# Optimization experiments

Measured on AMD Instinct MI355X. Metric: run time of the kernel, lower is better.

## Reference

```python
import jax, jax.numpy as jnp
import numpy as np

N_HEAD = 16
N_EMBD = 1024
B, T = 4, 1024


def setup_inputs() -> dict:
    key = jax.random.key(0)
    ks = jax.random.split(key, 8)
    hs = N_EMBD // N_HEAD
    x = jax.random.normal(ks[0], (B, T, N_EMBD), dtype=jnp.float32)
    # previous-layer attention load per token, ~O(1/T) like a softmax column mean
    refractory_state = jax.random.uniform(ks[1], (B, T), dtype=jnp.float32) / T
    s_attn = 1.0 / np.sqrt(N_EMBD)
    W_attn = jax.random.normal(ks[2], (N_EMBD, 3 * N_EMBD), dtype=jnp.float32) * s_attn
    b_attn = jnp.zeros((3 * N_EMBD,), dtype=jnp.float32)
    W_proj = jax.random.normal(ks[3], (N_EMBD, N_EMBD), dtype=jnp.float32) * s_attn
    b_proj = jnp.zeros((N_EMBD,), dtype=jnp.float32)
    # learnable LIF params, init per module (lif_mode='refractory')
    threshold = jnp.full((N_HEAD,), 0.01, dtype=jnp.float32)
    leak = jnp.full((N_HEAD,), 2.0, dtype=jnp.float32)
    steepness = jnp.full((N_HEAD,), 2.0, dtype=jnp.float32)
    ref_strength = jnp.full((N_HEAD,), -2.0, dtype=jnp.float32)
    cross_w = jnp.full((N_HEAD,), -2.0, dtype=jnp.float32)
    return {
        "x": x, "refractory_state": refractory_state,
        "W_attn": W_attn, "b_attn": b_attn,
        "W_proj": W_proj, "b_proj": b_proj,
        "threshold": threshold, "leak": leak, "steepness": steepness,
        "ref_strength": ref_strength, "cross_w": cross_w,
    }


def reference(x, refractory_state, W_attn, b_attn, W_proj, b_proj,
              threshold, leak, steepness, ref_strength, cross_w):
    Bq, Tq, C = x.shape
    H = N_HEAD
    hs = C // H
    qkv = x @ W_attn + b_attn                     # [B,T,3C]
    q, k, v = jnp.split(qkv, 3, axis=-1)
    q = q.reshape(Bq, Tq, H, hs).transpose(0, 2, 1, 3)  # [B,H,T,hs]
    k = k.reshape(Bq, Tq, H, hs).transpose(0, 2, 1, 3)
    v = v.reshape(Bq, Tq, H, hs).transpose(0, 2, 1, 3)

    att = jnp.einsum('bhqd,bhkd->bhqk', q, k) * (1.0 / jnp.sqrt(jnp.asarray(hs, x.dtype)))
    causal = jnp.tril(jnp.ones((Tq, Tq), dtype=bool))
    att = jnp.where(causal[None, None], att, -jnp.inf)
    probs = jax.nn.softmax(att, axis=-1)          # [B,H,T,T]

    thr = (jnp.abs(threshold) * 0.1)[None, :, None, None]
    lk = jax.nn.sigmoid(leak)[None, :, None, None]
    st = jax.nn.softplus(steepness)[None, :, None, None]
    # refractory: column load over queries + cross-layer load
    column_load = probs.mean(axis=-2, keepdims=True)          # [B,H,1,T]
    eff_thr = thr + jax.nn.softplus(ref_strength)[None, :, None, None] * column_load
    eff_thr = eff_thr + jax.nn.sigmoid(cross_w)[None, :, None, None] * refractory_state[:, None, None, :]

    fire = jax.nn.sigmoid(st * (probs - eff_thr))
    lif_w = fire + lk * (1.0 - fire)
    mod = probs * lif_w
    mod = mod / (mod.sum(axis=-1, keepdims=True) + 1e-8)
    new_refractory = mod.mean(axis=1).mean(axis=-2)           # [B,T]

    y = jnp.einsum('bhqk,bhkd->bhqd', mod, v)
    y = y.transpose(0, 2, 1, 3).reshape(Bq, Tq, C)
    y = y @ W_proj + b_proj
    return y, new_refractory
```

## Files before the change

### kernel.cpp

```cpp
#include <hip/hip_runtime.h>
#include <math.h>

#define B_  4
#define T_  1024
#define C_  1024
#define H_  16
#define HS_ 64
#define K2E 0.1803368801f
#define LOG2E 1.44269504f

typedef _Float16 f16;
typedef _Float16 f16x8 __attribute__((ext_vector_type(8)));
typedef float f32x4 __attribute__((ext_vector_type(4)));

#define MFMA16(a,b,c) __builtin_amdgcn_mfma_f32_16x16x32_f16(a,b,c,0,0,0)
#define EXP2(x) __builtin_amdgcn_exp2f(x)
#define RCP(x)  __builtin_amdgcn_rcpf(x)

__device__ __forceinline__ float qsum_(float v){
    v += __shfl_xor(v,1,64); v += __shfl_xor(v,2,64);
    v += __shfl_xor(v,4,64); v += __shfl_xor(v,8,64);
    return v;
}
__device__ __forceinline__ float sigmoidf_(float x){ return 1.0f/(1.0f + __expf(-x)); }
__device__ __forceinline__ float softplusf_(float x){ return fmaxf(x, 0.0f) + log1pf(__expf(-fabsf(x))); }

__global__ __launch_bounds__(256) void conv_f16_k(
    const float* __restrict__ in, f16* __restrict__ out, int n8)
{
    int i = blockIdx.x*256 + threadIdx.x;
    if (i < n8){
        const float4* p = (const float4*)in + (size_t)i*2;
        float4 a = p[0], b = p[1];
        f16x8 o;
        o[0]=(f16)a.x; o[1]=(f16)a.y; o[2]=(f16)a.z; o[3]=(f16)a.w;
        o[4]=(f16)b.x; o[5]=(f16)b.y; o[6]=(f16)b.z; o[7]=(f16)b.w;
        *((f16x8*)out + i) = o;
    }
}

__global__ __launch_bounds__(256) void transpose_f16_k(
    const float* __restrict__ in, f16* __restrict__ out, int K, int N)
{
    __shared__ float tl[32][33];
    const int n0 = blockIdx.x*32, k0 = blockIdx.y*32;
    const int c = threadIdx.x & 31, r4 = threadIdx.x >> 5;
    #pragma unroll
    for (int i=0;i<4;i++){
        int r = r4*4 + i;
        tl[r][c] = in[(size_t)(k0+r)*N + n0 + c];
    }
    __syncthreads();
    #pragma unroll
    for (int i=0;i<4;i++){
        int r = r4*4 + i;
        out[(size_t)(n0+r)*K + k0 + c] = (f16)tl[c][r];
    }
}

__global__ __launch_bounds__(256) void gemm_qkv_k(
    const f16* __restrict__ A, const f16* __restrict__ Bt,
    const float* __restrict__ bias,
    f16* __restrict__ Qh, f16* __restrict__ Kh, f16* __restrict__ Vt)
{
    __shared__ __align__(16) f16 Al[4*1032];
    __shared__ __align__(16) f16 Bl[4*1032];
    const int tid = threadIdx.x;
    const int lane = tid & 63, wave = tid >> 6;
    const int lx = lane & 15, quad = lane >> 4;
    const int wm = wave & 1, wn = wave >> 1;
    const int m0 = blockIdx.y*128, n0 = blockIdx.x*128;
    f32x4 acc[4][4];
    #pragma unroll
    for (int i=0;i<4;i++){
        #pragma unroll
        for (int j=0;j<4;j++){ acc[i][j][0]=0.f;acc[i][j][1]=0.f;acc[i][j][2]=0.f;acc[i][j][3]=0.f; }
    }
    for (int k0=0; k0<1024; k0+=32){
        __syncthreads();
        #pragma unroll
        for (int i=0;i<2;i++){
            int g = i*256 + tid;
            int m = g >> 2, kc = g & 3;
            *(f16x8*)&Al[kc*1032 + m*8] = *(const f16x8*)(A  + (size_t)(m0+m)*1024 + k0 + kc*8);
            *(f16x8*)&Bl[kc*1032 + m*8] = *(const f16x8*)(Bt + (size_t)(n0+m)*1024 + k0 + kc*8);
        }
        __syncthreads();
        f16x8 af[4], bf[4];
        #pragma unroll
        for (int mt=0;mt<4;mt++) af[mt] = *(const f16x8*)&Al[quad*1032 + (wm*64+mt*16+lx)*8];
        #pragma unroll
        for (int nt=0;nt<4;nt++) bf[nt] = *(const f16x8*)&Bl[quad*1032 + (wn*64+nt*16+lx)*8];
        #pragma unroll
        for (int mt=0;mt<4;mt++){
            #pragma unroll
            for (int nt=0;nt<4;nt++)
                acc[mt][nt] = MFMA16(af[mt], bf[nt], acc[mt][nt]);
        }
    }
    #pragma unroll
    for (int mt=0;mt<4;mt++){
        #pragma unroll
        for (int nt=0;nt<4;nt++){
            int n = n0 + wn*64 + nt*16 + lx;
            int which = n >> 10, cc = n & 1023, h = cc >> 6, d = cc & 63;
            float bv = bias[n];
            #pragma unroll
            for (int r=0;r<4;r++){
                int m = m0 + wm*64 + mt*16 + quad*4 + r;
                int bb = m >> 10, t = m & 1023;
                int bh = bb*16 + h;
                float v = acc[mt][nt][r] + bv;
                if (which==0)      Qh[((size_t)bh*1024 + t)*64 + d] = (f16)v;
                else if (which==1) Kh[((size_t)bh*1024 + t)*64 + d] = (f16)v;
                else               Vt[((size_t)bh*64 + d)*1024 + t] = (f16)v;
            }
        }
    }
}

__global__ __launch_bounds__(256) void gemm_proj_k(
    const f16* __restrict__ A, const f16* __restrict__ Bt,
    const float* __restrict__ bias, float* __restrict__ out)
{
    __shared__ __align__(16) f16 Al[4*1032];
    __shared__ __align__(16) f16 Bl[4*1032];
    const int tid = threadIdx.x;
    const int lane = tid & 63, wave = tid >> 6;
    const int lx = lane & 15, quad = lane >> 4;
    const int wm = wave & 1, wn = wave >> 1;
    const int m0 = blockIdx.y*128, n0 = blockIdx.x*128;
    f32x4 acc[4][4];
    #pragma unroll
    for (int i=0;i<4;i++){
        #pragma unroll
        for (int j=0;j<4;j++){ acc[i][j][0]=0.f;acc[i][j][1]=0.f;acc[i][j][2]=0.f;acc[i][j][3]=0.f; }
    }
    for (int k0=0; k0<1024; k0+=32){
        __syncthreads();
        #pragma unroll
        for (int i=0;i<2;i++){
            int g = i*256 + tid;
            int m = g >> 2, kc = g & 3;
            *(f16x8*)&Al[kc*1032 + m*8] = *(const f16x8*)(A  + (size_t)(m0+m)*1024 + k0 + kc*8);
            *(f16x8*)&Bl[kc*1032 + m*8] = *(const f16x8*)(Bt + (size_t)(n0+m)*1024 + k0 + kc*8);
        }
        __syncthreads();
        f16x8 af[4], bf[4];
        #pragma unroll
        for (int mt=0;mt<4;mt++) af[mt] = *(const f16x8*)&Al[quad*1032 + (wm*64+mt*16+lx)*8];
        #pragma unroll
        for (int nt=0;nt<4;nt++) bf[nt] = *(const f16x8*)&Bl[quad*1032 + (wn*64+nt*16+lx)*8];
        #pragma unroll
        for (int mt=0;mt<4;mt++){
            #pragma unroll
            for (int nt=0;nt<4;nt++)
                acc[mt][nt] = MFMA16(af[mt], bf[nt], acc[mt][nt]);
        }
    }
    #pragma unroll
    for (int mt=0;mt<4;mt++){
        #pragma unroll
        for (int nt=0;nt<4;nt++){
            int n = n0 + wn*64 + nt*16 + lx;
            float bv = bias[n];
            #pragma unroll
            for (int r=0;r<4;r++){
                int m = m0 + wm*64 + mt*16 + quad*4 + r;
                out[(size_t)m*1024 + n] = acc[mt][nt][r] + bv;
            }
        }
    }
}

__global__ __launch_bounds__(256) void attn_stats_k(
    const f16* __restrict__ Qh, const f16* __restrict__ Kh,
    float* __restrict__ rowl, float* __restrict__ colp)
{
    __shared__ __align__(16) f16 Kl[8*520];
    __shared__ float colacc[64];
    const int tid = threadIdx.x;
    const int lane = tid & 63, wave = tid >> 6;
    const int lx = lane & 15, quad = lane >> 4;
    const int pair = blockIdx.x >> 6;
    const int bh = blockIdx.x & 63;
    const int qpos = wave*16 + quad*4;

    #pragma unroll 1
    for (int gi=0; gi<2; gi++){
        const int g = gi ? (15-pair) : pair;
        const size_t qoff = ((size_t)bh*1024 + g*64 + wave*16 + lx)*64;
        f16x8 aq0 = *(const f16x8*)(Qh + qoff + quad*8);
        f16x8 aq1 = *(const f16x8*)(Qh + qoff + 32 + quad*8);

        float ls[4] = {0.f,0.f,0.f,0.f};
        for (int kt=0; kt<=g; kt++){
            __syncthreads();
            #pragma unroll
            for (int i=0;i<2;i++){
                int gix = i*256 + tid;
                int key = gix >> 3, kc = gix & 7;
                *(f16x8*)&Kl[kc*520 + key*8] =
                    *(const f16x8*)(Kh + ((size_t)bh*1024 + kt*64 + key)*64 + kc*8);
            }
            __syncthreads();
            const bool diag = (kt == g);
            #pragma unroll
            for (int nt=0;nt<4;nt++){
                f32x4 sc = {0.f,0.f,0.f,0.f};
                f16x8 b0 = *(const f16x8*)&Kl[quad*520     + (nt*16+lx)*8];
                f16x8 b1 = *(const f16x8*)&Kl[(4+quad)*520 + (nt*16+lx)*8];
                sc = MFMA16(aq0, b0, sc);
                sc = MFMA16(aq1, b1, sc);
                #pragma unroll
                for (int r=0;r<4;r++){
                    float sv = sc[r];
                    if (diag && (nt*16+lx) > (qpos + r)) sv = -1e4f;
                    ls[r] += EXP2(sv*K2E);
                }
            }
        }
        float invl[4];
        #pragma unroll
        for (int r=0;r<4;r++){
            float l = qsum_(ls[r]);
            if (lx == 0) rowl[(size_t)bh*1024 + g*64 + qpos + r] = l;
            invl[r] = RCP(l);
        }

        for (int kt=0; kt<=g; kt++){
            __syncthreads();
            #pragma unroll
            for (int i=0;i<2;i++){
                int gix = i*256 + tid;
                int key = gix >> 3, kc = gix & 7;
                *(f16x8*)&Kl[kc*520 + key*8] =
                    *(const f16x8*)(Kh + ((size_t)bh*1024 + kt*64 + key)*64 + kc*8);
            }
            if (tid < 64) colacc[tid] = 0.f;
            __syncthreads();
            const bool diag = (kt == g);
            #pragma unroll
            for (int nt=0;nt<4;nt++){
                f32x4 sc = {0.f,0.f,0.f,0.f};
                f16x8 b0 = *(const f16x8*)&Kl[quad*520     + (nt*16+lx)*8];
                f16x8 b1 = *(const f16x8*)&Kl[(4+quad)*520 + (nt*16+lx)*8];
                sc = MFMA16(aq0, b0, sc);
                sc = MFMA16(aq1, b1, sc);
                float csum = 0.f;
                #pragma unroll
                for (int r=0;r<4;r++){
                    float sv = sc[r];
                    if (diag && (nt*16+lx) > (qpos + r)) sv = -1e4f;
                    csum += EXP2(sv*K2E) * invl[r];
                }
                csum += __shfl_xor(csum,16,64); csum += __shfl_xor(csum,32,64);
                if (quad == 0) atomicAdd(&colacc[nt*16+lx], csum);
            }
            __syncthreads();
            if (tid < 64) atomicAdd(&colp[(size_t)bh*1024 + kt*64 + tid], colacc[tid]);
        }
    }
}

__global__ __launch_bounds__(256) void attn_apply_k(
    const f16* __restrict__ Qh, const f16* __restrict__ Kh, const f16* __restrict__ Vt,
    const float* __restrict__ rowl,
    const float* __restrict__ colp, const float* __restrict__ refr,
    const float* __restrict__ threshold, const float* __restrict__ leak,
    const float* __restrict__ steepness, const float* __restrict__ ref_strength,
    const float* __restrict__ cross_w,
    f16* __restrict__ Yh, float* __restrict__ racc)
{
    __shared__ __align__(16) f16 Kl[8*520];
    __shared__ __align__(16) f16 Vl[8*520];
    __shared__ __align__(16) f16 Pl[4][16*72];
    __shared__ float eb[1024];
    __shared__ float colacc[64];
    const int tid = threadIdx.x;
    const int lane = tid & 63, wave = tid >> 6;
    const int lx = lane & 15, quad = lane >> 4;
    const int pair = blockIdx.x >> 6;
    const int bh = blockIdx.x & 63;
    const int b  = bh >> 4, h = bh & 15;
    const int qpos = wave*16 + quad*4;

    const float thr = fabsf(threshold[h])*0.1f;
    const float lk  = sigmoidf_(leak[h]);
    const float st2 = softplusf_(steepness[h]) * LOG2E;
    const float sprT= softplusf_(ref_strength[h]) * (1.0f/T_);
    const float cw  = sigmoidf_(cross_w[h]);
    const float Alk = 1.f - lk;

    {
        float4 cp = *(const float4*)(colp + (size_t)bh*1024 + tid*4);
        float4 rf = *(const float4*)(refr + (size_t)b*1024 + tid*4);
        eb[tid*4+0] = thr + sprT*cp.x + cw*rf.x;
        eb[tid*4+1] = thr + sprT*cp.y + cw*rf.y;
        eb[tid*4+2] = thr + sprT*cp.z + cw*rf.z;
        eb[tid*4+3] = thr + sprT*cp.w + cw*rf.w;
    }

    #pragma unroll 1
    for (int gi=0; gi<2; gi++){
        const int g = gi ? (15-pair) : pair;
        const size_t qoff = ((size_t)bh*1024 + g*64 + wave*16 + lx)*64;
        f16x8 aq0 = *(const f16x8*)(Qh + qoff + quad*8);
        f16x8 aq1 = *(const f16x8*)(Qh + qoff + 32 + quad*8);

        float invl[4];
        #pragma unroll
        for (int r=0;r<4;r++)
            invl[r] = RCP(rowl[(size_t)bh*1024 + g*64 + qpos + r]);

        f32x4 y[4];
        #pragma unroll
        for (int i=0;i<4;i++){ y[i][0]=0.f;y[i][1]=0.f;y[i][2]=0.f;y[i][3]=0.f; }
        float Dp[4] = {0.f,0.f,0.f,0.f};

        for (int kt=0; kt<=g; kt++){
            __syncthreads();
            #pragma unroll
            for (int i=0;i<2;i++){
                int gix = i*256 + tid;
                int key = gix >> 3, kc = gix & 7;
                *(f16x8*)&Kl[kc*520 + key*8] =
                    *(const f16x8*)(Kh + ((size_t)bh*1024 + kt*64 + key)*64 + kc*8);
                *(f16x8*)&Vl[kc*520 + key*8] =
                    *(const f16x8*)(Vt + ((size_t)bh*64 + key)*1024 + kt*64 + kc*8);
            }
            __syncthreads();
            const bool diag = (kt == g);
            #pragma unroll
            for (int nt=0;nt<4;nt++){
                f32x4 sc = {0.f,0.f,0.f,0.f};
                f16x8 b0 = *(const f16x8*)&Kl[quad*520     + (nt*16+lx)*8];
                f16x8 b1 = *(const f16x8*)&Kl[(4+quad)*520 + (nt*16+lx)*8];
                sc = MFMA16(aq0, b0, sc);
                sc = MFMA16(aq1, b1, sc);
                float ec = st2 * eb[kt*64 + nt*16 + lx];
                #pragma unroll
                for (int r=0;r<4;r++){
                    float sv = sc[r];
                    if (diag && (nt*16+lx) > (qpos + r)) sv = -1e4f;
                    float p = EXP2(sv*K2E) * invl[r];
                    float e2 = EXP2(ec - st2*p);
                    float fire = RCP(1.f + e2);
                    float pw = p * (lk + Alk*fire);
                    Dp[r] += pw;
                    Pl[wave][(quad*4+r)*72 + nt*16 + lx] = (f16)pw;
                }
            }
            __syncthreads();
            f16x8 ap0 = *(const f16x8*)&Pl[wave][lx*72 + quad*8];
            f16x8 ap1 = *(const f16x8*)&Pl[wave][lx*72 + 32 + quad*8];
            #pragma unroll
            for (int dt=0;dt<4;dt++){
                f16x8 bv0 = *(const f16x8*)&Vl[quad*520     + (dt*16+lx)*8];
                f16x8 bv1 = *(const f16x8*)&Vl[(4+quad)*520 + (dt*16+lx)*8];
                y[dt] = MFMA16(ap0, bv0, y[dt]);
                y[dt] = MFMA16(ap1, bv1, y[dt]);
            }
        }
        float invD[4];
        #pragma unroll
        for (int r=0;r<4;r++) invD[r] = RCP(qsum_(Dp[r]) + 1e-8f);
        #pragma unroll
        for (int dt=0;dt<4;dt++){
            #pragma unroll
            for (int r=0;r<4;r++){
                Yh[(size_t)(b*1024 + g*64 + wave*16 + quad*4 + r)*1024 + h*64 + dt*16 + lx]
                    = (f16)(y[dt][r]*invD[r]);
            }
        }

        for (int kt=0; kt<=g; kt++){
            __syncthreads();
            #pragma unroll
            for (int i=0;i<2;i++){
                int gix = i*256 + tid;
                int key = gix >> 3, kc = gix & 7;
                *(f16x8*)&Kl[kc*520 + key*8] =
                    *(const f16x8*)(Kh + ((size_t)bh*1024 + kt*64 + key)*64 + kc*8);
            }
            if (tid < 64) colacc[tid] = 0.f;
            __syncthreads();
            const bool diag = (kt == g);
            #pragma unroll
            for (int nt=0;nt<4;nt++){
                f32x4 sc = {0.f,0.f,0.f,0.f};
                f16x8 b0 = *(const f16x8*)&Kl[quad*520     + (nt*16+lx)*8];
                f16x8 b1 = *(const f16x8*)&Kl[(4+quad)*520 + (nt*16+lx)*8];
                sc = MFMA16(aq0, b0, sc);
                sc = MFMA16(aq1, b1, sc);
                float ec = st2 * eb[kt*64 + nt*16 + lx];
                float csum = 0.f;
                #pragma unroll
                for (int r=0;r<4;r++){
                    float sv = sc[r];
                    if (diag && (nt*16+lx) > (qpos + r)) sv = -1e4f;
                    float p = EXP2(sv*K2E) * invl[r];
                    float e2 = EXP2(ec - st2*p);
                    float fire = RCP(1.f + e2);
                    csum += p * (lk + Alk*fire) * invD[r];
                }
                csum += __shfl_xor(csum,16,64); csum += __shfl_xor(csum,32,64);
                if (quad == 0) atomicAdd(&colacc[nt*16+lx], csum);
            }
            __syncthreads();
            if (tid < 64) atomicAdd(&racc[(size_t)b*1024 + kt*64 + tid], colacc[tid]);
        }
    }
}

__global__ __launch_bounds__(256) void finish_refr_k(
    const float* __restrict__ racc, float* __restrict__ out)
{
    int i = blockIdx.x*256 + threadIdx.x;
    if (i < B_*T_) out[i] = racc[i] * (1.0f/(H_*T_));
}

extern "C" void kernel_launch(void* const* d_in, const int* in_sizes, int n_in,
                              void* d_out, int out_size, void* d_ws, size_t ws_size,
                              hipStream_t stream) {
    (void)in_sizes; (void)n_in; (void)out_size; (void)ws_size;
    const float* x           = (const float*)d_in[0];
    const float* refr        = (const float*)d_in[1];
    const float* W_attn      = (const float*)d_in[2];
    const float* b_attn      = (const float*)d_in[3];
    const float* W_proj      = (const float*)d_in[4];
    const float* b_proj      = (const float*)d_in[5];
    const float* threshold   = (const float*)d_in[6];
    const float* leak        = (const float*)d_in[7];
    const float* steepness   = (const float*)d_in[8];
    const float* ref_strength= (const float*)d_in[9];
    const float* cross_w     = (const float*)d_in[10];
    float* out = (float*)d_out;

    char* ws = (char*)d_ws;
    f16* x_h = (f16*)ws;                       ws += (size_t)4096*1024*2;
    f16* WaT = (f16*)ws;                       ws += (size_t)3072*1024*2;
    f16* WpT = (f16*)ws;                       ws += (size_t)1024*1024*2;
    f16* Qh  = (f16*)ws;                       ws += (size_t)64*1024*64*2;
    f16* Kh  = (f16*)ws;                       ws += (size_t)64*1024*64*2;
    f16* Vt  = (f16*)ws;                       ws += (size_t)64*64*1024*2;
    f16* Yh  = (f16*)ws;                       ws += (size_t)4096*1024*2;
    float* rowl = (float*)ws;                  ws += (size_t)65536*4;
    float* colp = (float*)ws;                  ws += (size_t)65536*4;
    float* racc = (float*)ws;                  ws += (size_t)4096*4;

    hipMemsetAsync(colp, 0, 65536*sizeof(float), stream);
    hipMemsetAsync(racc, 0, 4096*sizeof(float), stream);

    conv_f16_k<<<dim3(2048), dim3(256), 0, stream>>>(x, x_h, 4096*1024/8);
    transpose_f16_k<<<dim3(96,32), dim3(256), 0, stream>>>(W_attn, WaT, 1024, 3072);
    transpose_f16_k<<<dim3(32,32), dim3(256), 0, stream>>>(W_proj, WpT, 1024, 1024);
    gemm_qkv_k<<<dim3(24,32), dim3(256), 0, stream>>>(x_h, WaT, b_attn, Qh, Kh, Vt);
    attn_stats_k<<<dim3(512), dim3(256), 0, stream>>>(Qh, Kh, rowl, colp);
    attn_apply_k<<<dim3(512), dim3(256), 0, stream>>>(
        Qh, Kh, Vt, rowl, colp, refr,
        threshold, leak, steepness, ref_strength, cross_w, Yh, racc);
    gemm_proj_k<<<dim3(8,32), dim3(256), 0, stream>>>(Yh, WpT, b_proj, out);
    finish_refr_k<<<dim3(16), dim3(256), 0, stream>>>(racc, out + (size_t)B_*T_*C_);
}
```

Measured before the change: 313.9 us.

## Use direct global-to-LDS loads, split attention blocks, narrow proj GEMM tiles

Result: no change. 319.1 us (+1.7%).

```diff
diff --git a/kernel.cpp b/kernel.cpp
--- a/kernel.cpp
+++ b/kernel.cpp
@@ -16,6 +16,12 @@
 #define MFMA16(a,b,c) __builtin_amdgcn_mfma_f32_16x16x32_f16(a,b,c,0,0,0)
 #define EXP2(x) __builtin_amdgcn_exp2f(x)
 #define RCP(x)  __builtin_amdgcn_rcpf(x)
+
+__device__ __forceinline__ void gload16(const f16* g, f16* l){
+    __builtin_amdgcn_global_load_lds(
+        (const __attribute__((address_space(1))) void*)g,
+        (__attribute__((address_space(3))) void*)l, 16, 0, 0);
+}
 
 __device__ __forceinline__ float qsum_(float v){
     v += __shfl_xor(v,1,64); v += __shfl_xor(v,2,64);
@@ -63,8 +69,8 @@
     const float* __restrict__ bias,
     f16* __restrict__ Qh, f16* __restrict__ Kh, f16* __restrict__ Vt)
 {
-    __shared__ __align__(16) f16 Al[4*1032];
-    __shared__ __align__(16) f16 Bl[4*1032];
+    __shared__ __align__(16) f16 Al[8*512];
+    __shared__ __align__(16) f16 Bl[8*512];
     const int tid = threadIdx.x;
     const int lane = tid & 63, wave = tid >> 6;
     const int lx = lane & 15, quad = lane >> 4;
@@ -80,17 +86,16 @@
         __syncthreads();
         #pragma unroll
         for (int i=0;i<2;i++){
-            int g = i*256 + tid;
-            int m = g >> 2, kc = g & 3;
-            *(f16x8*)&Al[kc*1032 + m*8] = *(const f16x8*)(A  + (size_t)(m0+m)*1024 + k0 + kc*8);
-            *(f16x8*)&Bl[kc*1032 + m*8] = *(const f16x8*)(Bt + (size_t)(n0+m)*1024 + k0 + kc*8);
+            int c = i*4 + wave;
+            gload16(A  + (size_t)(m0 + c*16 + lx)*1024 + k0 + quad*8, &Al[c*512]);
+            gload16(Bt + (size_t)(n0 + c*16 + lx)*1024 + k0 + quad*8, &Bl[c*512]);
         }
         __syncthreads();
         f16x8 af[4], bf[4];
         #pragma unroll
-        for (int mt=0;mt<4;mt++) af[mt] = *(const f16x8*)&Al[quad*1032 + (wm*64+mt*16+lx)*8];
-        #pragma unroll
-        for (int nt=0;nt<4;nt++) bf[nt] = *(const f16x8*)&Bl[quad*1032 + (wn*64+nt*16+lx)*8];
+        for (int mt=0;mt<4;mt++) af[mt] = *(const f16x8*)&Al[(wm*4+mt)*512 + quad*128 + lx*8];
+        #pragma unroll
+        for (int nt=0;nt<4;nt++) bf[nt] = *(const f16x8*)&Bl[(wn*4+nt)*512 + quad*128 + lx*8];
         #pragma unroll
         for (int mt=0;mt<4;mt++){
             #pragma unroll
@@ -123,46 +128,47 @@
     const f16* __restrict__ A, const f16* __restrict__ Bt,
     const float* __restrict__ bias, float* __restrict__ out)
 {
-    __shared__ __align__(16) f16 Al[4*1032];
-    __shared__ __align__(16) f16 Bl[4*1032];
+    __shared__ __align__(16) f16 Al[8*512];
+    __shared__ __align__(16) f16 Bl[4*512];
     const int tid = threadIdx.x;
     const int lane = tid & 63, wave = tid >> 6;
     const int lx = lane & 15, quad = lane >> 4;
     const int wm = wave & 1, wn = wave >> 1;
-    const int m0 = blockIdx.y*128, n0 = blockIdx.x*128;
-    f32x4 acc[4][4];
+    const int m0 = blockIdx.y*128, n0 = blockIdx.x*64;
+    f32x4 acc[4][2];
     #pragma unroll
     for (int i=0;i<4;i++){
         #pragma unroll
-        for (int j=0;j<4;j++){ acc[i][j][0]=0.f;acc[i][j][1]=0.f;acc[i][j][2]=0.f;acc[i][j][3]=0.f; }
+        for (int j=0;j<2;j++){ acc[i][j][0]=0.f;acc[i][j][1]=0.f;acc[i][j][2]=0.f;acc[i][j][3]=0.f; }
     }
     for (int k0=0; k0<1024; k0+=32){
         __syncthreads();
         #pragma unroll
-        for (int i=0;i<2;i++){
-            int g = i*256 + tid;
-            int m = g >> 2, kc = g & 3;
-            *(f16x8*)&Al[kc*1032 + m*8] = *(const f16x8*)(A  + (size_t)(m0+m)*1024 + k0 + kc*8);
-            *(f16x8*)&Bl[kc*1032 + m*8] = *(const f16x8*)(Bt + (size_t)(n0+m)*1024 + k0 + kc*8);
-        }
-        __syncthreads();
-        f16x8 af[4], bf[4];
-        #pragma unroll
-        for (int mt=0;mt<4;mt++) af[mt] = *(const f16x8*)&Al[quad*1032 + (wm*64+mt*16+lx)*8];
-        #pragma unroll
-        for (int nt=0;nt<4;nt++) bf[nt] = *(const f16x8*)&Bl[quad*1032 + (wn*64+nt*16+lx)*8];
+        for (int i=0;i<3;i++){
+            int u = i*4 + wave;
+            if (u < 8)
+                gload16(A  + (size_t)(m0 + u*16 + lx)*1024 + k0 + quad*8, &Al[u*512]);
+            else
+                gload16(Bt + (size_t)(n0 + (u-8)*16 + lx)*1024 + k0 + quad*8, &Bl[(u-8)*512]);
+        }
+        __syncthreads();
+        f16x8 af[4], bf[2];
+        #pragma unroll
+        for (int mt=0;mt<4;mt++) af[mt] = *(const f16x8*)&Al[(wm*4+mt)*512 + quad*128 + lx*8];
+        #pragma unroll
+        for (int nt=0;nt<2;nt++) bf[nt] = *(const f16x8*)&Bl[(wn*2+nt)*512 + quad*128 + lx*8];
         #pragma unroll
         for (int mt=0;mt<4;mt++){
             #pragma unroll
-            for (int nt=0;nt<4;nt++)
+            for (int nt=0;nt<2;nt++)
                 acc[mt][nt] = MFMA16(af[mt], bf[nt], acc[mt][nt]);
         }
     }
     #pragma unroll
     for (int mt=0;mt<4;mt++){
         #pragma unroll
-        for (int nt=0;nt<4;nt++){
-            int n = n0 + wn*64 + nt*16 + lx;
+        for (int nt=0;nt<2;nt++){
+            int n = n0 + wn*32 + nt*16 + lx;
             float bv = bias[n];
             #pragma unroll
             for (int r=0;r<4;r++){
@@ -177,89 +183,83 @@
     const f16* __restrict__ Qh, const f16* __restrict__ Kh,
     float* __restrict__ rowl, float* __restrict__ colp)
 {
-    __shared__ __align__(16) f16 Kl[8*520];
+    __shared__ __align__(16) f16 Kl[4096];
     __shared__ float colacc[64];
     const int tid = threadIdx.x;
     const int lane = tid & 63, wave = tid >> 6;
     const int lx = lane & 15, quad = lane >> 4;
-    const int pair = blockIdx.x >> 6;
+    const int g  = 15 - (blockIdx.x >> 6);
     const int bh = blockIdx.x & 63;
     const int qpos = wave*16 + quad*4;
 
-    #pragma unroll 1
-    for (int gi=0; gi<2; gi++){
-        const int g = gi ? (15-pair) : pair;
-        const size_t qoff = ((size_t)bh*1024 + g*64 + wave*16 + lx)*64;
-        f16x8 aq0 = *(const f16x8*)(Qh + qoff + quad*8);
-        f16x8 aq1 = *(const f16x8*)(Qh + qoff + 32 + quad*8);
-
-        float ls[4] = {0.f,0.f,0.f,0.f};
-        for (int kt=0; kt<=g; kt++){
-            __syncthreads();
-            #pragma unroll
-            for (int i=0;i<2;i++){
-                int gix = i*256 + tid;
-                int key = gix >> 3, kc = gix & 7;
-                *(f16x8*)&Kl[kc*520 + key*8] =
-                    *(const f16x8*)(Kh + ((size_t)bh*1024 + kt*64 + key)*64 + kc*8);
-            }
-            __syncthreads();
-            const bool diag = (kt == g);
-            #pragma unroll
-            for (int nt=0;nt<4;nt++){
-                f32x4 sc = {0.f,0.f,0.f,0.f};
-                f16x8 b0 = *(const f16x8*)&Kl[quad*520     + (nt*16+lx)*8];
-                f16x8 b1 = *(const f16x8*)&Kl[(4+quad)*520 + (nt*16+lx)*8];
-                sc = MFMA16(aq0, b0, sc);
-                sc = MFMA16(aq1, b1, sc);
-                #pragma unroll
-                for (int r=0;r<4;r++){
-                    float sv = sc[r];
-                    if (diag && (nt*16+lx) > (qpos + r)) sv = -1e4f;
-                    ls[r] += EXP2(sv*K2E);
-                }
-            }
-        }
-        float invl[4];
-        #pragma unroll
-        for (int r=0;r<4;r++){
-            float l = qsum_(ls[r]);
-            if (lx == 0) rowl[(size_t)bh*1024 + g*64 + qpos + r] = l;
-            invl[r] = RCP(l);
-        }
-
-        for (int kt=0; kt<=g; kt++){
-            __syncthreads();
-            #pragma unroll
-            for (int i=0;i<2;i++){
-                int gix = i*256 + tid;
-                int key = gix >> 3, kc = gix & 7;
-                *(f16x8*)&Kl[kc*520 + key*8] =
-                    *(const f16x8*)(Kh + ((size_t)bh*1024 + kt*64 + key)*64 + kc*8);
-            }
-            if (tid < 64) colacc[tid] = 0.f;
-            __syncthreads();
-            const bool diag = (kt == g);
-            #pragma unroll
-            for (int nt=0;nt<4;nt++){
-                f32x4 sc = {0.f,0.f,0.f,0.f};
-                f16x8 b0 = *(const f16x8*)&Kl[quad*520     + (nt*16+lx)*8];
-                f16x8 b1 = *(const f16x8*)&Kl[(4+quad)*520 + (nt*16+lx)*8];
-                sc = MFMA16(aq0, b0, sc);
-                sc = MFMA16(aq1, b1, sc);
-                float csum = 0.f;
-                #pragma unroll
-                for (int r=0;r<4;r++){
-                    float sv = sc[r];
-                    if (diag && (nt*16+lx) > (qpos + r)) sv = -1e4f;
-                    csum += EXP2(sv*K2E) * invl[r];
-                }
-                csum += __shfl_xor(csum,16,64); csum += __shfl_xor(csum,32,64);
-                if (quad == 0) atomicAdd(&colacc[nt*16+lx], csum);
-            }
-            __syncthreads();
-            if (tid < 64) atomicAdd(&colp[(size_t)bh*1024 + kt*64 + tid], colacc[tid]);
-        }
+    const size_t qoff = ((size_t)bh*1024 + g*64 + wave*16 + lx)*64;
+    f16x8 aq0 = *(const f16x8*)(Qh + qoff + quad*8);
+    f16x8 aq1 = *(const f16x8*)(Qh + qoff + 32 + quad*8);
+
+    float ls[4] = {0.f,0.f,0.f,0.f};
+    for (int kt=0; kt<=g; kt++){
+        __syncthreads();
+        #pragma unroll
+        for (int i=0;i<2;i++){
+            int u = i*4 + wave, c = u & 3, kh = u >> 2;
+            gload16(Kh + ((size_t)bh*1024 + kt*64 + c*16 + lx)*64 + kh*32 + quad*8,
+                    &Kl[c*1024 + kh*512]);
+        }
+        __syncthreads();
+        const bool diag = (kt == g);
+        #pragma unroll
+        for (int nt=0;nt<4;nt++){
+            f32x4 sc = {0.f,0.f,0.f,0.f};
+            f16x8 b0 = *(const f16x8*)&Kl[nt*1024 + quad*128 + lx*8];
+            f16x8 b1 = *(const f16x8*)&Kl[nt*1024 + (4+quad)*128 + lx*8];
+            sc = MFMA16(aq0, b0, sc);
+            sc = MFMA16(aq1, b1, sc);
+            #pragma unroll
+            for (int r=0;r<4;r++){
+                float sv = sc[r];
+                if (diag && (nt*16+lx) > (qpos + r)) sv = -1e4f;
+                ls[r] += EXP2(sv*K2E);
+            }
+        }
+    }
+    float invl[4];
+    #pragma unroll
+    for (int r=0;r<4;r++){
+        float l = qsum_(ls[r]);
+        if (lx == 0) rowl[(size_t)bh*1024 + g*64 + qpos + r] = l;
+        invl[r] = RCP(l);
+    }
+
+    for (int kt=0; kt<=g; kt++){
+        __syncthreads();
+        #pragma unroll
+        for (int i=0;i<2;i++){
+            int u = i*4 + wave, c = u & 3, kh = u >> 2;
+            gload16(Kh + ((size_t)bh*1024 + kt*64 + c*16 + lx)*64 + kh*32 + quad*8,
+                    &Kl[c*1024 + kh*512]);
+        }
+        if (tid < 64) colacc[tid] = 0.f;
+        __syncthreads();
+        const bool diag = (kt == g);
+        #pragma unroll
+        for (int nt=0;nt<4;nt++){
+            f32x4 sc = {0.f,0.f,0.f,0.f};
+            f16x8 b0 = *(const f16x8*)&Kl[nt*1024 + quad*128 + lx*8];
+            f16x8 b1 = *(const f16x8*)&Kl[nt*1024 + (4+quad)*128 + lx*8];
+            sc = MFMA16(aq0, b0, sc);
+            sc = MFMA16(aq1, b1, sc);
+            float csum = 0.f;
+            #pragma unroll
+            for (int r=0;r<4;r++){
+                float sv = sc[r];
+                if (diag && (nt*16+lx) > (qpos + r)) sv = -1e4f;
+                csum += EXP2(sv*K2E) * invl[r];
+            }
+            csum += __shfl_xor(csum,16,64); csum += __shfl_xor(csum,32,64);
+            if (quad == 0) atomicAdd(&colacc[nt*16+lx], csum);
+        }
+        __syncthreads();
+        if (tid < 64) atomicAdd(&colp[(size_t)bh*1024 + kt*64 + tid], colacc[tid]);
     }
 }
 
@@ -272,15 +272,15 @@
     const float* __restrict__ cross_w,
     f16* __restrict__ Yh, float* __restrict__ racc)
 {
-    __shared__ __align__(16) f16 Kl[8*520];
-    __shared__ __align__(16) f16 Vl[8*520];
+    __shared__ __align__(16) f16 Kl[4096];
+    __shared__ __align__(16) f16 Vl[4096];
     __shared__ __align__(16) f16 Pl[4][16*72];
     __shared__ float eb[1024];
     __shared__ float colacc[64];
     const int tid = threadIdx.x;
     const int lane = tid & 63, wave = tid >> 6;
     const int lx = lane & 15, quad = lane >> 4;
-    const int pair = blockIdx.x >> 6;
+    const int g  = 15 - (blockIdx.x >> 6);
     const int bh = blockIdx.x & 63;
     const int b  = bh >> 4, h = bh & 15;
     const int qpos = wave*16 + quad*4;
@@ -301,115 +301,113 @@
         eb[tid*4+3] = thr + sprT*cp.w + cw*rf.w;
     }
 
-    #pragma unroll 1
-    for (int gi=0; gi<2; gi++){
-        const int g = gi ? (15-pair) : pair;
-        const size_t qoff = ((size_t)bh*1024 + g*64 + wave*16 + lx)*64;
-        f16x8 aq0 = *(const f16x8*)(Qh + qoff + quad*8);
-        f16x8 aq1 = *(const f16x8*)(Qh + qoff + 32 + quad*8);
-
-        float invl[4];
-        #pragma unroll
-        for (int r=0;r<4;r++)
-            invl[r] = RCP(rowl[(size_t)bh*1024 + g*64 + qpos + r]);
-
-        f32x4 y[4];
-        #pragma unroll
-        for (int i=0;i<4;i++){ y[i][0]=0.f;y[i][1]=0.f;y[i][2]=0.f;y[i][3]=0.f; }
-        float Dp[4] = {0.f,0.f,0.f,0.f};
-
-        for (int kt=0; kt<=g; kt++){
-            __syncthreads();
-            #pragma unroll
-            for (int i=0;i<2;i++){
-                int gix = i*256 + tid;
-                int key = gix >> 3, kc = gix & 7;
-                *(f16x8*)&Kl[kc*520 + key*8] =
-                    *(const f16x8*)(Kh + ((size_t)bh*1024 + kt*64 + key)*64 + kc*8);
-                *(f16x8*)&Vl[kc*520 + key*8] =
-                    *(const f16x8*)(Vt + ((size_t)bh*64 + key)*1024 + kt*64 + kc*8);
-            }
-            __syncthreads();
-            const bool diag = (kt == g);
-            #pragma unroll
-            for (int nt=0;nt<4;nt++){
-                f32x4 sc = {0.f,0.f,0.f,0.f};
-                f16x8 b0 = *(const f16x8*)&Kl[quad*520     + (nt*16+lx)*8];
-                f16x8 b1 = *(const f16x8*)&Kl[(4+quad)*520 + (nt*16+lx)*8];
-                sc = MFMA16(aq0, b0, sc);
-                sc = MFMA16(aq1, b1, sc);
-                float ec = st2 * eb[kt*64 + nt*16 + lx];
-                #pragma unroll
-                for (int r=0;r<4;r++){
-                    float sv = sc[r];
-                    if (diag && (nt*16+lx) > (qpos + r)) sv = -1e4f;
-                    float p = EXP2(sv*K2E) * invl[r];
-                    float e2 = EXP2(ec - st2*p);
-                    float fire = RCP(1.f + e2);
-                    float pw = p * (lk + Alk*fire);
-                    Dp[r] += pw;
-                    Pl[wave][(quad*4+r)*72 + nt*16 + lx] = (f16)pw;
-                }
-            }
-            __syncthreads();
-            f16x8 ap0 = *(const f16x8*)&Pl[wave][lx*72 + quad*8];
-            f16x8 ap1 = *(const f16x8*)&Pl[wave][lx*72 + 32 + quad*8];
-            #pragma unroll
-            for (int dt=0;dt<4;dt++){
-                f16x8 bv0 = *(const f16x8*)&Vl[quad*520     + (dt*16+lx)*8];
-                f16x8 bv1 = *(const f16x8*)&Vl[(4+quad)*520 + (dt*16+lx)*8];
-                y[dt] = MFMA16(ap0, bv0, y[dt]);
-                y[dt] = MFMA16(ap1, bv1, y[dt]);
-            }
-        }
-        float invD[4];
-        #pragma unroll
-        for (int r=0;r<4;r++) invD[r] = RCP(qsum_(Dp[r]) + 1e-8f);
+    const size_t qoff = ((size_t)bh*1024 + g*64 + wave*16 + lx)*64;
+    f16x8 aq0 = *(const f16x8*)(Qh + qoff + quad*8);
+    f16x8 aq1 = *(const f16x8*)(Qh + qoff + 32 + quad*8);
+
+    float invl[4];
+    #pragma unroll
+    for (int r=0;r<4;r++)
+        invl[r] = RCP(rowl[(size_t)bh*1024 + g*64 + qpos + r]);
+
+    f32x4 y[4];
+    #pragma unroll
+    for (int i=0;i<4;i++){ y[i][0]=0.f;y[i][1]=0.f;y[i][2]=0.f;y[i][3]=0.f; }
+    float Dp[4] = {0.f,0.f,0.f,0.f};
+
+    for (int kt=0; kt<=g; kt++){
+        __syncthreads();
+        #pragma unroll
+        for (int i=0;i<4;i++){
+            int u = i*4 + wave;
+            if (u < 8){
+                int c = u & 3, kh = u >> 2;
+                gload16(Kh + ((size_t)bh*1024 + kt*64 + c*16 + lx)*64 + kh*32 + quad*8,
+                        &Kl[c*1024 + kh*512]);
+            } else {
+                int v = u - 8, c = v & 3, kh = v >> 2;
+                gload16(Vt + ((size_t)bh*64 + c*16 + lx)*1024 + kt*64 + kh*32 + quad*8,
+                        &Vl[c*1024 + kh*512]);
+            }
+        }
+        __syncthreads();
+        const bool diag = (kt == g);
+        #pragma unroll
+        for (int nt=0;nt<4;nt++){
+            f32x4 sc = {0.f,0.f,0.f,0.f};
+            f16x8 b0 = *(const f16x8*)&Kl[nt*1024 + quad*128 + lx*8];
+            f16x8 b1 = *(const f16x8*)&Kl[nt*1024 + (4+quad)*128 + lx*8];
+            sc = MFMA16(aq0, b0, sc);
+            sc = MFMA16(aq1, b1, sc);
+            float ec = st2 * eb[kt*64 + nt*16 + lx];
+            #pragma unroll
+            for (int r=0;r<4;r++){
+                float sv = sc[r];
+                if (diag && (nt*16+lx) > (qpos + r)) sv = -1e4f;
+                float p = EXP2(sv*K2E) * invl[r];
+                float e2 = EXP2(ec - st2*p);
+                float fire = RCP(1.f + e2);
+                float pw = p * (lk + Alk*fire);
+                Dp[r] += pw;
+                Pl[wave][(quad*4+r)*72 + nt*16 + lx] = (f16)pw;
+            }
+        }
+        f16x8 ap0 = *(const f16x8*)&Pl[wave][lx*72 + quad*8];
+        f16x8 ap1 = *(const f16x8*)&Pl[wave][lx*72 + 32 + quad*8];
         #pragma unroll
         for (int dt=0;dt<4;dt++){
-            #pragma unroll
-            for (int r=0;r<4;r++){
-                Yh[(size_t)(b*1024 + g*64 + wave*16 + quad*4 + r)*1024 + h*64 + dt*16 + lx]
-                    = (f16)(y[dt][r]*invD[r]);
-            }
-        }
-
-        for (int kt=0; kt<=g; kt++){
-            __syncthreads();
-            #pragma unroll
-            for (int i=0;i<2;i++){
-                int gix = i*256 + tid;
-                int key = gix >> 3, kc = gix & 7;
-                *(f16x8*)&Kl[kc*520 + key*8] =
-                    *(const f16x8*)(Kh + ((size_t)bh*1024 + kt*64 + key)*64 + kc*8);
-            }
-            if (tid < 64) colacc[tid] = 0.f;
-            __syncthreads();
-            const bool diag = (kt == g);
-            #pragma unroll
-            for (int nt=0;nt<4;nt++){
-                f32x4 sc = {0.f,0.f,0.f,0.f};
-                f16x8 b0 = *(const f16x8*)&Kl[quad*520     + (nt*16+lx)*8];
-                f16x8 b1 = *(const f16x8*)&Kl[(4+quad)*520 + (nt*16+lx)*8];
-                sc = MFMA16(aq0, b0, sc);
-                sc = MFMA16(aq1, b1, sc);
-                float ec = st2 * eb[kt*64 + nt*16 + lx];
-                float csum = 0.f;
-                #pragma unroll
-                for (int r=0;r<4;r++){
-                    float sv = sc[r];
-                    if (diag && (nt*16+lx) > (qpos + r)) sv = -1e4f;
-                    float p = EXP2(sv*K2E) * invl[r];
-                    float e2 = EXP2(ec - st2*p);
-                    float fire = RCP(1.f + e2);
-                    csum += p * (lk + Alk*fire) * invD[r];
-                }
-                csum += __shfl_xor(csum,16,64); csum += __shfl_xor(csum,32,64);
-                if (quad == 0) atomicAdd(&colacc[nt*16+lx], csum);
-            }
-            __syncthreads();
-            if (tid < 64) atomicAdd(&racc[(size_t)b*1024 + kt*64 + tid], colacc[tid]);
-        }
+            f16x8 bv0 = *(const f16x8*)&Vl[dt*1024 + quad*128 + lx*8];
+            f16x8 bv1 = *(const f16x8*)&Vl[dt*1024 + (4+quad)*128 + lx*8];
+            y[dt] = MFMA16(ap0, bv0, y[dt]);
+            y[dt] = MFMA16(ap1, bv1, y[dt]);
+        }
+    }
+    float invD[4];
+    #pragma unroll
+    for (int r=0;r<4;r++) invD[r] = RCP(qsum_(Dp[r]) + 1e-8f);
+    #pragma unroll
+    for (int dt=0;dt<4;dt++){
+        #pragma unroll
+        for (int r=0;r<4;r++){
+            Yh[(size_t)(b*1024 + g*64 + wave*16 + quad*4 + r)*1024 + h*64 + dt*16 + lx]
+                = (f16)(y[dt][r]*invD[r]);
+        }
+    }
+
+    for (int kt=0; kt<=g; kt++){
+        __syncthreads();
+        #pragma unroll
+        for (int i=0;i<2;i++){
+            int u = i*4 + wave, c = u & 3, kh = u >> 2;
+            gload16(Kh + ((size_t)bh*1024 + kt*64 + c*16 + lx)*64 + kh*32 + quad*8,
+                    &Kl[c*1024 + kh*512]);
+        }
+        if (tid < 64) colacc[tid] = 0.f;
+        __syncthreads();
+        const bool diag = (kt == g);
+        #pragma unroll
+        for (int nt=0;nt<4;nt++){
+            f32x4 sc = {0.f,0.f,0.f,0.f};
+            f16x8 b0 = *(const f16x8*)&Kl[nt*1024 + quad*128 + lx*8];
+            f16x8 b1 = *(const f16x8*)&Kl[nt*1024 + (4+quad)*128 + lx*8];
+            sc = MFMA16(aq0, b0, sc);
+            sc = MFMA16(aq1, b1, sc);
+            float ec = st2 * eb[kt*64 + nt*16 + lx];
+            float csum = 0.f;
+            #pragma unroll
+            for (int r=0;r<4;r++){
+                float sv = sc[r];
+                if (diag && (nt*16+lx) > (qpos + r)) sv = -1e4f;
+                float p = EXP2(sv*K2E) * invl[r];
+                float e2 = EXP2(ec - st2*p);
+                float fire = RCP(1.f + e2);
+                csum += p * (lk + Alk*fire) * invD[r];
+            }
+            csum += __shfl_xor(csum,16,64); csum += __shfl_xor(csum,32,64);
+            if (quad == 0) atomicAdd(&colacc[nt*16+lx], csum);
+        }
+        __syncthreads();
+        if (tid < 64) atomicAdd(&racc[(size_t)b*1024 + kt*64 + tid], colacc[tid]);
     }
 }
 
@@ -456,10 +454,10 @@
     transpose_f16_k<<<dim3(96,32), dim3(256), 0, stream>>>(W_attn, WaT, 1024, 3072);
     transpose_f16_k<<<dim3(32,32), dim3(256), 0, stream>>>(W_proj, WpT, 1024, 1024);
     gemm_qkv_k<<<dim3(24,32), dim3(256), 0, stream>>>(x_h, WaT, b_attn, Qh, Kh, Vt);
-    attn_stats_k<<<dim3(512), dim3(256), 0, stream>>>(Qh, Kh, rowl, colp);
-    attn_apply_k<<<dim3(512), dim3(256), 0, stream>>>(
+    attn_stats_k<<<dim3(1024), dim3(256), 0, stream>>>(Qh, Kh, rowl, colp);
+    attn_apply_k<<<dim3(1024), dim3(256), 0, stream>>>(
         Qh, Kh, Vt, rowl, colp, refr,
         threshold, leak, steepness, ref_strength, cross_w, Yh, racc);
-    gemm_proj_k<<<dim3(8,32), dim3(256), 0, stream>>>(Yh, WpT, b_proj, out);
+    gemm_proj_k<<<dim3(16,32), dim3(256), 0, stream>>>(Yh, WpT, b_proj, out);
     finish_refr_k<<<dim3(16), dim3(256), 0, stream>>>(racc, out + (size_t)B_*T_*C_);
 }
```
